# Performance work log

Measured on AMD Instinct MI355X. Metric: run time of the kernel, lower is better.

## Reference

```python
import jax, jax.numpy as jnp
import numpy as np

N_NODES = 100000
N_EDGES = 1600000
IN_F = 256
OUT_F = 128


def setup_inputs() -> dict:
    key = jax.random.key(0)
    k1, k2, k3, k4, k5, k6 = jax.random.split(key, 6)
    init_range = float(np.sqrt(6.0 / (IN_F + OUT_F)))
    stdv = 1.0 / float(np.sqrt(OUT_F))
    return {
        "x": jax.random.normal(k1, (N_NODES, IN_F), dtype=jnp.float32),
        "weight": jax.random.uniform(k2, (IN_F, OUT_F), dtype=jnp.float32, minval=-init_range, maxval=init_range),
        "bias": jax.random.uniform(k3, (OUT_F,), dtype=jnp.float32, minval=-stdv, maxval=stdv),
        "adj_val": jax.random.uniform(k4, (N_EDGES,), dtype=jnp.float32),
        "adj_row": jax.random.randint(k5, (N_EDGES,), 0, N_NODES),  # destination node per edge
        "adj_col": jax.random.randint(k6, (N_EDGES,), 0, N_NODES),  # source node per edge
    }


def reference(x, weight, bias, adj_val, adj_row, adj_col):
    # support = X @ W   (dense GEMM, [N, in] x [in, out])
    support = x @ weight
    # output = spmm(adj, support): gather source rows, scale by edge value,
    # segment-sum into destination rows. Honors COO sparsity; no [N,N] dense.
    gathered = support[adj_col] * adj_val[:, None]          # [E, out]
    out = jax.ops.segment_sum(gathered, adj_row, num_segments=N_NODES)
    return out + bias
```

## Files before the change

### kernel.cpp

```cpp
#include <hip/hip_runtime.h>

#define N_NODES 100000
#define N_EDGES 1600000
#define IN_F 256
#define OUT_F 128

#define NBUCK 391
#define NCHUNK 256
#define CHUNK_E (N_EDGES / NCHUNK)
#define NSCAN (NBUCK * NCHUNK)
#define SCAN_BLK 4096
#define NSCAN_BLOCKS ((NSCAN + SCAN_BLK - 1) / SCAN_BLK)

#define GEMM_BM 128
#define GEMM_BLOCKS ((N_NODES + GEMM_BM - 1) / GEMM_BM)

typedef __attribute__((ext_vector_type(8))) short bf16x8;
typedef __attribute__((ext_vector_type(4))) float f32x4;

__device__ __forceinline__ unsigned short f2bf(float f) {
    unsigned u = __float_as_uint(f);
    unsigned r = u + 0x7fffu + ((u >> 16) & 1u);
    return (unsigned short)(r >> 16);
}

__global__ __launch_bounds__(256) void count_wtrans_kernel(const int* __restrict__ rowi,
                                                           int* __restrict__ counts,
                                                           const float* __restrict__ w,
                                                           unsigned short* __restrict__ wt) {
    const int tid = threadIdx.x;
    if (blockIdx.x >= NCHUNK) {
        int c = blockIdx.x - NCHUNK;
        wt[c * IN_F + tid] = f2bf(w[tid * OUT_F + c]);
        return;
    }
    __shared__ int hist[NBUCK];
    const int c = blockIdx.x;
    for (int i = tid; i < NBUCK; i += 256) hist[i] = 0;
    __syncthreads();
    const int e0 = c * CHUNK_E;
    for (int i = tid; i < CHUNK_E; i += 256)
        atomicAdd(&hist[rowi[e0 + i] >> 8], 1);
    __syncthreads();
    for (int i = tid; i < NBUCK; i += 256) counts[i * NCHUNK + c] = hist[i];
}

__global__ __launch_bounds__(256) void scan1_kernel(int* __restrict__ data,
                                                    int* __restrict__ blocksums,
                                                    int n) {
    __shared__ int sdata[256];
    const int tid = threadIdx.x;
    const int base = blockIdx.x * SCAN_BLK + tid * 16;
    int v[16];
    if (base < n) {
#pragma unroll
        for (int q = 0; q < 4; ++q) {
            int4 t = *reinterpret_cast<const int4*>(&data[base + q * 4]);
            v[q * 4 + 0] = t.x; v[q * 4 + 1] = t.y; v[q * 4 + 2] = t.z; v[q * 4 + 3] = t.w;
        }
    } else {
#pragma unroll
        for (int i = 0; i < 16; ++i) v[i] = 0;
    }
    int pre[16], run = 0;
#pragma unroll
    for (int i = 0; i < 16; ++i) { pre[i] = run; run += v[i]; }
    sdata[tid] = run;
    __syncthreads();
#pragma unroll
    for (int off = 1; off < 256; off <<= 1) {
        int t = (tid >= off) ? sdata[tid - off] : 0;
        __syncthreads();
        sdata[tid] += t;
        __syncthreads();
    }
    int excl = (tid == 0) ? 0 : sdata[tid - 1];
    if (base < n) {
#pragma unroll
        for (int q = 0; q < 4; ++q) {
            int4 t = {excl + pre[q * 4 + 0], excl + pre[q * 4 + 1],
                      excl + pre[q * 4 + 2], excl + pre[q * 4 + 3]};
            *reinterpret_cast<int4*>(&data[base + q * 4]) = t;
        }
    }
    if (tid == 255) blocksums[blockIdx.x] = sdata[255];
}

__global__ __launch_bounds__(256) void scan2_kernel(int* __restrict__ blocksums, int nblk) {
    __shared__ int sdata[256];
    const int tid = threadIdx.x;
    sdata[tid] = (tid < nblk) ? blocksums[tid] : 0;
    __syncthreads();
#pragma unroll
    for (int off = 1; off < 256; off <<= 1) {
        int t = (tid >= off) ? sdata[tid - off] : 0;
        __syncthreads();
        sdata[tid] += t;
        __syncthreads();
    }
    if (tid < nblk) blocksums[tid] = (tid == 0) ? 0 : sdata[tid - 1];
}

__global__ __launch_bounds__(512, 4) void gemm_scatter_kernel(const float* __restrict__ x,
                                                              const unsigned short* __restrict__ wt,
                                                              unsigned short* __restrict__ support,
                                                              const int* __restrict__ rowi,
                                                              const int* __restrict__ coli,
                                                              const float* __restrict__ val,
                                                              const int* __restrict__ counts,
                                                              const int* __restrict__ blocksums,
                                                              uint2* __restrict__ tmp) {
    __shared__ unsigned short ws[128 * 256];
    __shared__ int cur[NBUCK];

    const int tid = threadIdx.x;

    if (blockIdx.x < NCHUNK) {
        const int c = blockIdx.x;
        for (int i = tid; i < NBUCK; i += 512) {
            int j = i * NCHUNK + c;
            cur[i] = counts[j] + blocksums[j >> 12];
        }
        __syncthreads();
        const int e0 = c * CHUNK_E;
        for (int i = tid; i < CHUNK_E; i += 512) {
            int e = e0 + i;
            int dst = rowi[e];
            int b = dst >> 8;
            int pos = atomicAdd(&cur[b], 1);
            tmp[pos] = make_uint2(((unsigned)(dst & 255) << 17) | (unsigned)coli[e],
                                  __float_as_uint(val[e]));
        }
        return;
    }

    const int lane = tid & 63;
    const int wv = tid >> 6;
    const int row0 = (blockIdx.x - NCHUNK) * GEMM_BM;
    const int l15 = lane & 15;
    const int kq = lane >> 4;

#pragma unroll
    for (int it = 0; it < 8; ++it) {
        int ci = it * 512 + tid;
        int col = ci >> 5, ch = ci & 31;
        uint4 v = *reinterpret_cast<const uint4*>(&wt[col * IN_F + ch * 8]);
        int slot = ch ^ (col & 7);
        *reinterpret_cast<uint4*>(&ws[col * 256 + slot * 8]) = v;
    }
    __syncthreads();

    int arow = row0 + wv * 16 + l15;
    if (arow > N_NODES - 1) arow = N_NODES - 1;
    const float* xrow = &x[(size_t)arow * IN_F + kq * 8];

    f32x4 acc[8];
#pragma unroll
    for (int n = 0; n < 8; ++n) acc[n] = (f32x4){0.f, 0.f, 0.f, 0.f};

#pragma unroll
    for (int kt = 0; kt < 8; ++kt) {
        f32x4 a0 = *reinterpret_cast<const f32x4*>(xrow + kt * 32);
        f32x4 a1 = *reinterpret_cast<const f32x4*>(xrow + kt * 32 + 4);
        bf16x8 af;
        af[0] = (short)f2bf(a0[0]); af[1] = (short)f2bf(a0[1]);
        af[2] = (short)f2bf(a0[2]); af[3] = (short)f2bf(a0[3]);
        af[4] = (short)f2bf(a1[0]); af[5] = (short)f2bf(a1[1]);
        af[6] = (short)f2bf(a1[2]); af[7] = (short)f2bf(a1[3]);
#pragma unroll
        for (int n = 0; n < 8; ++n) {
            int col = n * 16 + l15;
            int slot = (kt * 4 + kq) ^ (col & 7);
            bf16x8 bfv = *reinterpret_cast<const bf16x8*>(&ws[col * 256 + slot * 8]);
            acc[n] = __builtin_amdgcn_mfma_f32_16x16x32_bf16(af, bfv, acc[n], 0, 0, 0);
        }
    }

#pragma unroll
    for (int r = 0; r < 4; ++r) {
        int row = row0 + wv * 16 + kq * 4 + r;
        if (row < N_NODES) {
#pragma unroll
            for (int n = 0; n < 8; ++n) {
                support[(size_t)row * OUT_F + n * 16 + l15] = f2bf(acc[n][r]);
            }
        }
    }
}

__global__ __launch_bounds__(256) void fine_kernel(const uint2* __restrict__ tmp,
                                                   const int* __restrict__ counts,
                                                   const int* __restrict__ blocksums,
                                                   uint2* __restrict__ pairs,
                                                   int* __restrict__ offsets) {
    __shared__ int hist[256];
    __shared__ int scanb[256];
    __shared__ int cur[256];
    const int tid = threadIdx.x, b = blockIdx.x;
    int j0 = b * NCHUNK;
    const int start = counts[j0] + blocksums[j0 >> 12];
    int end;
    if (b == NBUCK - 1) end = N_EDGES;
    else {
        int j1 = (b + 1) * NCHUNK;
        end = counts[j1] + blocksums[j1 >> 12];
    }

    hist[tid] = 0;
    __syncthreads();
    for (int i = start + tid; i < end; i += 256)
        atomicAdd(&hist[tmp[i].x >> 17], 1);
    __syncthreads();
    int h = hist[tid];
    scanb[tid] = h;
    __syncthreads();
#pragma unroll
    for (int off = 1; off < 256; off <<= 1) {
        int t = (tid >= off) ? scanb[tid - off] : 0;
        __syncthreads();
        scanb[tid] += t;
        __syncthreads();
    }
    cur[tid] = start + scanb[tid] - h;
    int node = (b << 8) + tid;
    if (node < N_NODES) offsets[node] = start + scanb[tid];
    __syncthreads();
    for (int i = start + tid; i < end; i += 256) {
        uint2 u = tmp[i];
        int dl = u.x >> 17;
        int pos = atomicAdd(&cur[dl], 1);
        pairs[pos] = make_uint2(u.x & 0x1FFFFu, u.y);
    }
}

__global__ __launch_bounds__(256) void accum_kernel(const unsigned short* __restrict__ support,
                                                    const uint2* __restrict__ pairs,
                                                    const int* __restrict__ offsets,
                                                    const float* __restrict__ bias,
                                                    float* __restrict__ out) {
    const int node = blockIdx.x * 4 + (threadIdx.x >> 6);
    const int lane = threadIdx.x & 63;
    const int grp = lane >> 4;
    const int l16 = lane & 15;
    if (node >= N_NODES) return;

    const int start = (node == 0) ? 0 : offsets[node - 1];
    const int end = offsets[node];

    float acc[8];
#pragma unroll
    for (int t = 0; t < 8; ++t) acc[t] = 0.f;

    int j = start + grp;
    for (; j + 4 < end; j += 8) {
        uint2 p0 = pairs[j];
        uint2 p1 = pairs[j + 4];
        uint4 s0 = *reinterpret_cast<const uint4*>(&support[(size_t)p0.x * OUT_F + l16 * 8]);
        uint4 s1 = *reinterpret_cast<const uint4*>(&support[(size_t)p1.x * OUT_F + l16 * 8]);
        float v0 = __uint_as_float(p0.y);
        float v1 = __uint_as_float(p1.y);
        unsigned u0[4] = {s0.x, s0.y, s0.z, s0.w};
        unsigned u1[4] = {s1.x, s1.y, s1.z, s1.w};
#pragma unroll
        for (int q = 0; q < 4; ++q) {
            acc[2 * q + 0] += __uint_as_float(u0[q] << 16) * v0;
            acc[2 * q + 1] += __uint_as_float(u0[q] & 0xffff0000u) * v0;
            acc[2 * q + 0] += __uint_as_float(u1[q] << 16) * v1;
            acc[2 * q + 1] += __uint_as_float(u1[q] & 0xffff0000u) * v1;
        }
    }
    for (; j < end; j += 4) {
        uint2 p0 = pairs[j];
        uint4 s0 = *reinterpret_cast<const uint4*>(&support[(size_t)p0.x * OUT_F + l16 * 8]);
        float v0 = __uint_as_float(p0.y);
        unsigned u0[4] = {s0.x, s0.y, s0.z, s0.w};
#pragma unroll
        for (int q = 0; q < 4; ++q) {
            acc[2 * q + 0] += __uint_as_float(u0[q] << 16) * v0;
            acc[2 * q + 1] += __uint_as_float(u0[q] & 0xffff0000u) * v0;
        }
    }

#pragma unroll
    for (int t = 0; t < 8; ++t) {
        acc[t] += __shfl_xor(acc[t], 16);
        acc[t] += __shfl_xor(acc[t], 32);
    }

    if (grp == 0) {
        float4 b0 = *reinterpret_cast<const float4*>(&bias[l16 * 8]);
        float4 b1 = *reinterpret_cast<const float4*>(&bias[l16 * 8 + 4]);
        f32x4 o0 = {acc[0] + b0.x, acc[1] + b0.y, acc[2] + b0.z, acc[3] + b0.w};
        f32x4 o1 = {acc[4] + b1.x, acc[5] + b1.y, acc[6] + b1.z, acc[7] + b1.w};
        f32x4* op = reinterpret_cast<f32x4*>(&out[(size_t)node * OUT_F + l16 * 8]);
        __builtin_nontemporal_store(o0, op);
        __builtin_nontemporal_store(o1, op + 1);
    }
}

extern "C" void kernel_launch(void* const* d_in, const int* in_sizes, int n_in,
                              void* d_out, int out_size, void* d_ws, size_t ws_size,
                              hipStream_t stream) {
    const float* x       = (const float*)d_in[0];
    const float* weight  = (const float*)d_in[1];
    const float* bias    = (const float*)d_in[2];
    const float* adj_val = (const float*)d_in[3];
    const int*   adj_row = (const int*)d_in[4];
    const int*   adj_col = (const int*)d_in[5];
    float* out = (float*)d_out;

    unsigned short* support = (unsigned short*)d_ws;
    unsigned short* wt = support + (size_t)N_NODES * OUT_F;
    int* counts = (int*)(wt + IN_F * OUT_F);
    int* blocksums = counts + NSCAN;
    int* offsets = blocksums + 32;
    uint2* tmp = (uint2*)(offsets + 100000);
    uint2* pairs = tmp + N_EDGES;

    count_wtrans_kernel<<<NCHUNK + OUT_F, 256, 0, stream>>>(adj_row, counts, weight, wt);
    scan1_kernel<<<NSCAN_BLOCKS, 256, 0, stream>>>(counts, blocksums, NSCAN);
    scan2_kernel<<<1, 256, 0, stream>>>(blocksums, NSCAN_BLOCKS);
    gemm_scatter_kernel<<<NCHUNK + GEMM_BLOCKS, 512, 0, stream>>>(
        x, wt, support, adj_row, adj_col, adj_val, counts, blocksums, tmp);
    fine_kernel<<<NBUCK, 256, 0, stream>>>(tmp, counts, blocksums, pairs, offsets);
    accum_kernel<<<(N_NODES + 3) / 4, 256, 0, stream>>>(support, pairs, offsets, bias, out);
}
```

Measured before the change: 135.3 us.

## Fuse fine bucket sort into accumulation using LDS-resident edge lists

Shrinks coarse buckets to 64 destination nodes and fuses the fine sort with the gather-accumulate kernel, keeping per-bucket sorted edges in shared memory instead of writing pairs and offsets to global memory. This removes one kernel launch and a full global write/read of the edge list. The trade-offs are a larger prefix-scan over more buckets, lower parallelism in the accumulation phase, and a fixed LDS capacity per bucket with no overflow guard.

```diff
diff --git a/kernel.cpp b/kernel.cpp
--- a/kernel.cpp
+++ b/kernel.cpp
@@ -5,7 +5,7 @@
 #define IN_F 256
 #define OUT_F 128
 
-#define NBUCK 391
+#define NBUCK 1563
 #define NCHUNK 256
 #define CHUNK_E (N_EDGES / NCHUNK)
 #define NSCAN (NBUCK * NCHUNK)
@@ -14,6 +14,9 @@
 
 #define GEMM_BM 128
 #define GEMM_BLOCKS ((N_NODES + GEMM_BM - 1) / GEMM_BM)
+
+#define FBUCK 64
+#define CAP 1664
 
 typedef __attribute__((ext_vector_type(8))) short bf16x8;
 typedef __attribute__((ext_vector_type(4))) float f32x4;
@@ -40,7 +43,7 @@
     __syncthreads();
     const int e0 = c * CHUNK_E;
     for (int i = tid; i < CHUNK_E; i += 256)
-        atomicAdd(&hist[rowi[e0 + i] >> 8], 1);
+        atomicAdd(&hist[rowi[e0 + i] >> 6], 1);
     __syncthreads();
     for (int i = tid; i < NBUCK; i += 256) counts[i * NCHUNK + c] = hist[i];
 }
@@ -126,9 +129,9 @@
         for (int i = tid; i < CHUNK_E; i += 512) {
             int e = e0 + i;
             int dst = rowi[e];
-            int b = dst >> 8;
+            int b = dst >> 6;
             int pos = atomicAdd(&cur[b], 1);
-            tmp[pos] = make_uint2(((unsigned)(dst & 255) << 17) | (unsigned)coli[e],
+            tmp[pos] = make_uint2(((unsigned)(dst & 63) << 17) | (unsigned)coli[e],
                                   __float_as_uint(val[e]));
         }
         return;
@@ -188,14 +191,17 @@
     }
 }
 
-__global__ __launch_bounds__(256) void fine_kernel(const uint2* __restrict__ tmp,
-                                                   const int* __restrict__ counts,
-                                                   const int* __restrict__ blocksums,
-                                                   uint2* __restrict__ pairs,
-                                                   int* __restrict__ offsets) {
-    __shared__ int hist[256];
-    __shared__ int scanb[256];
-    __shared__ int cur[256];
+__global__ __launch_bounds__(256) void fine_accum_kernel(const unsigned short* __restrict__ support,
+                                                         const uint2* __restrict__ tmp,
+                                                         const int* __restrict__ counts,
+                                                         const int* __restrict__ blocksums,
+                                                         const float* __restrict__ bias,
+                                                         float* __restrict__ out) {
+    __shared__ uint2 plds[CAP];
+    __shared__ int hist[FBUCK];
+    __shared__ int scanb[FBUCK];
+    __shared__ int cur[FBUCK];
+
     const int tid = threadIdx.x, b = blockIdx.x;
     int j0 = b * NCHUNK;
     const int start = counts[j0] + blocksums[j0 >> 12];
@@ -206,95 +212,92 @@
         end = counts[j1] + blocksums[j1 >> 12];
     }
 
-    hist[tid] = 0;
+    if (tid < FBUCK) hist[tid] = 0;
     __syncthreads();
     for (int i = start + tid; i < end; i += 256)
         atomicAdd(&hist[tmp[i].x >> 17], 1);
     __syncthreads();
-    int h = hist[tid];
-    scanb[tid] = h;
-    __syncthreads();
-#pragma unroll
-    for (int off = 1; off < 256; off <<= 1) {
-        int t = (tid >= off) ? scanb[tid - off] : 0;
-        __syncthreads();
-        scanb[tid] += t;
-        __syncthreads();
-    }
-    cur[tid] = start + scanb[tid] - h;
-    int node = (b << 8) + tid;
-    if (node < N_NODES) offsets[node] = start + scanb[tid];
+    if (tid < FBUCK) scanb[tid] = hist[tid];
+    __syncthreads();
+#pragma unroll
+    for (int off = 1; off < FBUCK; off <<= 1) {
+        int t = (tid < FBUCK && tid >= off) ? scanb[tid - off] : 0;
+        __syncthreads();
+        if (tid < FBUCK) scanb[tid] += t;
+        __syncthreads();
+    }
+    if (tid < FBUCK) cur[tid] = scanb[tid] - hist[tid];
     __syncthreads();
     for (int i = start + tid; i < end; i += 256) {
         uint2 u = tmp[i];
         int dl = u.x >> 17;
         int pos = atomicAdd(&cur[dl], 1);
-        pairs[pos] = make_uint2(u.x & 0x1FFFFu, u.y);
-    }
-}
-
-__global__ __launch_bounds__(256) void accum_kernel(const unsigned short* __restrict__ support,
-                                                    const uint2* __restrict__ pairs,
-                                                    const int* __restrict__ offsets,
-                                                    const float* __restrict__ bias,
-                                                    float* __restrict__ out) {
-    const int node = blockIdx.x * 4 + (threadIdx.x >> 6);
-    const int lane = threadIdx.x & 63;
+        plds[pos] = make_uint2(u.x & 0x1FFFFu, u.y);
+    }
+    __syncthreads();
+
+    const int lane = tid & 63;
+    const int wv = tid >> 6;
     const int grp = lane >> 4;
     const int l16 = lane & 15;
-    if (node >= N_NODES) return;
-
-    const int start = (node == 0) ? 0 : offsets[node - 1];
-    const int end = offsets[node];
-
-    float acc[8];
-#pragma unroll
-    for (int t = 0; t < 8; ++t) acc[t] = 0.f;
-
-    int j = start + grp;
-    for (; j + 4 < end; j += 8) {
-        uint2 p0 = pairs[j];
-        uint2 p1 = pairs[j + 4];
-        uint4 s0 = *reinterpret_cast<const uint4*>(&support[(size_t)p0.x * OUT_F + l16 * 8]);
-        uint4 s1 = *reinterpret_cast<const uint4*>(&support[(size_t)p1.x * OUT_F + l16 * 8]);
-        float v0 = __uint_as_float(p0.y);
-        float v1 = __uint_as_float(p1.y);
-        unsigned u0[4] = {s0.x, s0.y, s0.z, s0.w};
-        unsigned u1[4] = {s1.x, s1.y, s1.z, s1.w};
-#pragma unroll
-        for (int q = 0; q < 4; ++q) {
-            acc[2 * q + 0] += __uint_as_float(u0[q] << 16) * v0;
-            acc[2 * q + 1] += __uint_as_float(u0[q] & 0xffff0000u) * v0;
-            acc[2 * q + 0] += __uint_as_float(u1[q] << 16) * v1;
-            acc[2 * q + 1] += __uint_as_float(u1[q] & 0xffff0000u) * v1;
-        }
-    }
-    for (; j < end; j += 4) {
-        uint2 p0 = pairs[j];
-        uint4 s0 = *reinterpret_cast<const uint4*>(&support[(size_t)p0.x * OUT_F + l16 * 8]);
-        float v0 = __uint_as_float(p0.y);
-        unsigned u0[4] = {s0.x, s0.y, s0.z, s0.w};
-#pragma unroll
-        for (int q = 0; q < 4; ++q) {
-            acc[2 * q + 0] += __uint_as_float(u0[q] << 16) * v0;
-            acc[2 * q + 1] += __uint_as_float(u0[q] & 0xffff0000u) * v0;
-        }
-    }
-
-#pragma unroll
-    for (int t = 0; t < 8; ++t) {
-        acc[t] += __shfl_xor(acc[t], 16);
-        acc[t] += __shfl_xor(acc[t], 32);
-    }
-
-    if (grp == 0) {
-        float4 b0 = *reinterpret_cast<const float4*>(&bias[l16 * 8]);
-        float4 b1 = *reinterpret_cast<const float4*>(&bias[l16 * 8 + 4]);
-        f32x4 o0 = {acc[0] + b0.x, acc[1] + b0.y, acc[2] + b0.z, acc[3] + b0.w};
-        f32x4 o1 = {acc[4] + b1.x, acc[5] + b1.y, acc[6] + b1.z, acc[7] + b1.w};
-        f32x4* op = reinterpret_cast<f32x4*>(&out[(size_t)node * OUT_F + l16 * 8]);
-        __builtin_nontemporal_store(o0, op);
-        __builtin_nontemporal_store(o1, op + 1);
+
+    float4 b0 = *reinterpret_cast<const float4*>(&bias[l16 * 8]);
+    float4 b1 = *reinterpret_cast<const float4*>(&bias[l16 * 8 + 4]);
+
+    for (int ni = 0; ni < 16; ++ni) {
+        const int dl = wv * 16 + ni;
+        const int node = b * FBUCK + dl;
+        if (node >= N_NODES) break;
+        const int s = (dl == 0) ? 0 : scanb[dl - 1];
+        const int e = scanb[dl];
+
+        float acc[8];
+#pragma unroll
+        for (int t = 0; t < 8; ++t) acc[t] = 0.f;
+
+        int j = s + grp;
+        for (; j + 4 < e; j += 8) {
+            uint2 p0 = plds[j];
+            uint2 p1 = plds[j + 4];
+            uint4 s0 = *reinterpret_cast<const uint4*>(&support[(size_t)p0.x * OUT_F + l16 * 8]);
+            uint4 s1 = *reinterpret_cast<const uint4*>(&support[(size_t)p1.x * OUT_F + l16 * 8]);
+            float v0 = __uint_as_float(p0.y);
+            float v1 = __uint_as_float(p1.y);
+            unsigned u0[4] = {s0.x, s0.y, s0.z, s0.w};
+            unsigned u1[4] = {s1.x, s1.y, s1.z, s1.w};
+#pragma unroll
+            for (int q = 0; q < 4; ++q) {
+                acc[2 * q + 0] += __uint_as_float(u0[q] << 16) * v0;
+                acc[2 * q + 1] += __uint_as_float(u0[q] & 0xffff0000u) * v0;
+                acc[2 * q + 0] += __uint_as_float(u1[q] << 16) * v1;
+                acc[2 * q + 1] += __uint_as_float(u1[q] & 0xffff0000u) * v1;
+            }
+        }
+        for (; j < e; j += 4) {
+            uint2 p0 = plds[j];
+            uint4 s0 = *reinterpret_cast<const uint4*>(&support[(size_t)p0.x * OUT_F + l16 * 8]);
+            float v0 = __uint_as_float(p0.y);
+            unsigned u0[4] = {s0.x, s0.y, s0.z, s0.w};
+#pragma unroll
+            for (int q = 0; q < 4; ++q) {
+                acc[2 * q + 0] += __uint_as_float(u0[q] << 16) * v0;
+                acc[2 * q + 1] += __uint_as_float(u0[q] & 0xffff0000u) * v0;
+            }
+        }
+
+#pragma unroll
+        for (int t = 0; t < 8; ++t) {
+            acc[t] += __shfl_xor(acc[t], 16);
+            acc[t] += __shfl_xor(acc[t], 32);
+        }
+
+        if (grp == 0) {
+            f32x4 o0 = {acc[0] + b0.x, acc[1] + b0.y, acc[2] + b0.z, acc[3] + b0.w};
+            f32x4 o1 = {acc[4] + b1.x, acc[5] + b1.y, acc[6] + b1.z, acc[7] + b1.w};
+            f32x4* op = reinterpret_cast<f32x4*>(&out[(size_t)node * OUT_F + l16 * 8]);
+            __builtin_nontemporal_store(o0, op);
+            __builtin_nontemporal_store(o1, op + 1);
+        }
     }
 }
 
@@ -313,15 +316,12 @@
     unsigned short* wt = support + (size_t)N_NODES * OUT_F;
     int* counts = (int*)(wt + IN_F * OUT_F);
     int* blocksums = counts + NSCAN;
-    int* offsets = blocksums + 32;
-    uint2* tmp = (uint2*)(offsets + 100000);
-    uint2* pairs = tmp + N_EDGES;
+    uint2* tmp = (uint2*)(blocksums + 128);
 
     count_wtrans_kernel<<<NCHUNK + OUT_F, 256, 0, stream>>>(adj_row, counts, weight, wt);
     scan1_kernel<<<NSCAN_BLOCKS, 256, 0, stream>>>(counts, blocksums, NSCAN);
     scan2_kernel<<<1, 256, 0, stream>>>(blocksums, NSCAN_BLOCKS);
     gemm_scatter_kernel<<<NCHUNK + GEMM_BLOCKS, 512, 0, stream>>>(
         x, wt, support, adj_row, adj_col, adj_val, counts, blocksums, tmp);
-    fine_kernel<<<NBUCK, 256, 0, stream>>>(tmp, counts, blocksums, pairs, offsets);
-    accum_kernel<<<(N_NODES + 3) / 4, 256, 0, stream>>>(support, pairs, offsets, bias, out);
-}
+    fine_accum_kernel<<<NBUCK, 256, 0, stream>>>(support, tmp, counts, blocksums, bias, out);
+}
```

Measured after the change: 127.5 us. -5.7%, faster.
